# Performance work log

Hardware: AMD Instinct MI355X
Metric: run time of the kernel (lower is better)

The kernel has to match this reference:

```python
import jax, jax.numpy as jnp
import numpy as np
import math

L = 6          # num_layers
D = 512        # hidden_dim
S = 2048       # seq_len
B = 8          # batch
ODIM = 1       # output_dim
SCALES = (24.0, 720.0)


def setup_inputs() -> dict:
    key = jax.random.key(0)
    ks = jax.random.split(key, 12)
    def n(k, shape, scale=0.02):
        return jax.random.normal(k, shape, dtype=jnp.float32) * scale
    return {
        "z": jax.random.normal(ks[0], (B, S, 1), dtype=jnp.float32),
        "c": jax.random.normal(ks[1], (B, S, 1), dtype=jnp.float32),
        "enc_w": n(ks[2], (D, 2)), "enc_b": jnp.zeros((D,), jnp.float32),
        "beta": jnp.ones((L, len(SCALES)), jnp.float32),
        "wq": n(ks[3], (L, D, D)), "bq": jnp.zeros((L, D), jnp.float32),
        "wk": n(ks[4], (L, D, D)), "bk": jnp.zeros((L, D), jnp.float32),
        "wv": n(ks[5], (L, D, D)), "bv": jnp.zeros((L, D), jnp.float32),
        "ln1_w": jnp.ones((L, D), jnp.float32), "ln1_b": jnp.zeros((L, D), jnp.float32),
        "ln2_w": jnp.ones((L, D), jnp.float32), "ln2_b": jnp.zeros((L, D), jnp.float32),
        "ff1_w": n(ks[6], (L, 4 * D, D)), "ff1_b": jnp.zeros((L, 4 * D), jnp.float32),
        "ff2_w": n(ks[7], (L, D, 4 * D)), "ff2_b": jnp.zeros((L, D), jnp.float32),
        "out_w": n(ks[8], (ODIM, D)), "out_b": jnp.zeros((ODIM,), jnp.float32),
    }


def _ln(x, w, b, eps=1e-5):
    m = jnp.mean(x, axis=-1, keepdims=True)
    v = jnp.var(x, axis=-1, keepdims=True)
    return (x - m) * jax.lax.rsqrt(v + eps) * w + b


def _posenc(seq_len, dim):
    pos = jnp.arange(seq_len, dtype=jnp.float32)[:, None]
    div = jnp.exp(jnp.arange(0, dim, 2, dtype=jnp.float32) * (-(math.log(10000.0) / dim)))
    pe = jnp.zeros((seq_len, dim), jnp.float32)
    pe = pe.at[:, 0::2].set(jnp.sin(pos * div))
    pe = pe.at[:, 1::2].set(jnp.cos(pos * div))
    return pe


def reference(z, c, enc_w, enc_b, beta, wq, bq, wk, bk, wv, bv,
              ln1_w, ln1_b, ln2_w, ln2_b, ff1_w, ff1_b, ff2_w, ff2_b,
              out_w, out_b):
    # SequenceEncoder: cat(z,c) -> Linear(2, D) -> + sinusoidal PE
    x = jnp.concatenate([z, c], axis=-1) @ enc_w.T + enc_b       # [B,S,D]
    seq_len, d = x.shape[1], x.shape[2]
    x = x + _posenc(seq_len, d)[None]
    sqrt_d = math.sqrt(d)

    idx = jnp.arange(seq_len, dtype=jnp.float32)
    dist = jnp.abs(idx[:, None] - idx[None, :])                  # [S,S]

    for l in range(L):
        # pre-norm with ln1 (applied twice in the original code - replicated)
        xn = _ln(x, ln1_w[l], ln1_b[l])
        Q = xn @ wq[l].T + bq[l]
        K = xn @ wk[l].T + bk[l]
        V = xn @ wv[l].T + bv[l]
        attn = jnp.einsum('bid,bjd->bij', Q, K) / sqrt_d          # [B,S,S]
        bias = beta[l, 0] * jnp.cos(2.0 * math.pi * dist / SCALES[0]) \
             + beta[l, 1] * jnp.cos(2.0 * math.pi * dist / SCALES[1])
        probs = jax.nn.softmax(attn + bias, axis=-1)
        att_out = jnp.einsum('bij,bjd->bid', probs, V)
        # original applies layer_norm_1 again to the residual sum
        x = _ln(x + att_out, ln1_w[l], ln1_b[l])
        xn2 = _ln(x, ln2_w[l], ln2_b[l])
        h = jax.nn.relu(xn2 @ ff1_w[l].T + ff1_b[l])
        x = x + h @ ff2_w[l].T + ff2_b[l]

    return x @ out_w.T + out_b                                    # [B,S,ODIM]
```

## Files before the change

kernel.cpp:

```cpp
#include <hip/hip_runtime.h>
#include <hip/hip_fp8.h>
#include <math.h>

#define BB 8
#define SS 2048
#define DD 512
#define LL 6
#define FFD 2048

typedef _Float16 half_t;
typedef __attribute__((ext_vector_type(8))) _Float16 half8;
typedef __attribute__((ext_vector_type(4))) float f32x4;

enum { EPI_NONE = 0, EPI_RELU = 2, EPI_RES = 3, EPI_ATTN = 4, EPI_QKV = 5, EPI_PV = 6 };

__device__ __forceinline__ unsigned char f2e4m3(float v) {
    __hip_fp8_e4m3 f(v);
    return f.__x;
}

__device__ __forceinline__ void gl_lds16(const void* g, void* l) {
    __builtin_amdgcn_global_load_lds(
        (const __attribute__((address_space(1))) unsigned int*)g,
        (__attribute__((address_space(3))) unsigned int*)l,
        16, 0, 0);
}

__device__ __forceinline__ void blockReduce2(float& a, float& b, float* sm) {
#pragma unroll
    for (int off = 32; off; off >>= 1) {
        a += __shfl_down(a, off);
        b += __shfl_down(b, off);
    }
    int lane = threadIdx.x & 63;
    int w = threadIdx.x >> 6;
    if (lane == 0) { sm[w] = a; sm[4 + w] = b; }
    __syncthreads();
    a = sm[0] + sm[1] + sm[2] + sm[3];
    b = sm[4] + sm[5] + sm[6] + sm[7];
    __syncthreads();
}

__global__ __launch_bounds__(256) void encode_kernel(
    const float* __restrict__ z, const float* __restrict__ c,
    const float* __restrict__ enc_w, const float* __restrict__ enc_b,
    float* __restrict__ x)
{
    int idx = blockIdx.x * 256 + threadIdx.x;
    int d  = idx & (DD - 1);
    int bs = idx >> 9;
    int s  = bs & (SS - 1);
    float v = z[bs] * enc_w[2 * d] + c[bs] * enc_w[2 * d + 1] + enc_b[d];
    float div = expf(-(float)(d & ~1) * (9.210340371976184f / 512.0f));
    float ang = (float)s * div;
    v += (d & 1) ? cosf(ang) : sinf(ang);
    x[idx] = v;
}

__global__ __launch_bounds__(256) void convert_layer_kernel(
    const float* __restrict__ wq, const float* __restrict__ wk,
    const float* __restrict__ wv, const float* __restrict__ f1,
    const float* __restrict__ f2, half_t* __restrict__ wqkv,
    half_t* __restrict__ f1h, half_t* __restrict__ f2h)
{
    const int NQ = DD * DD;
    int i = blockIdx.x * 256 + threadIdx.x;
    if (i < 3 * NQ) {
        int which = i >> 18, j = i & (NQ - 1);
        const float* s = (which == 0) ? wq : (which == 1) ? wk : wv;
        wqkv[i] = (half_t)s[j];
    } else {
        int k = i - 3 * NQ;
        if (k < FFD * DD) f1h[k] = (half_t)f1[k];
        else              f2h[k - FFD * DD] = (half_t)f2[k - FFD * DD];
    }
}

__global__ __launch_bounds__(256) void bias_table_kernel(
    const float* __restrict__ beta, float* __restrict__ tbl)
{
    int i = blockIdx.x * 256 + threadIdx.x;
    int l = i >> 11, d = i & (SS - 1);
    tbl[i] = beta[2 * l] * cosf(0.2617993877991494f * d)
           + beta[2 * l + 1] * cosf(0.008726646259971648f * d);
}

__global__ __launch_bounds__(256) void ln_kernel(
    const float* __restrict__ src, const float* __restrict__ w,
    const float* __restrict__ b, half_t* __restrict__ dst)
{
    __shared__ float sm[8];
    size_t row = blockIdx.x;
    const float* p = src + row * DD;
    int t = threadIdx.x;
    float v0 = p[t], v1 = p[t + 256];
    float s = v0 + v1, sq = v0 * v0 + v1 * v1;
    blockReduce2(s, sq, sm);
    float mean = s * (1.0f / DD);
    float var  = sq * (1.0f / DD) - mean * mean;
    float rs   = rsqrtf(var + 1e-5f);
    dst[row * DD + t]       = (half_t)((v0 - mean) * rs * w[t] + b[t]);
    dst[row * DD + t + 256] = (half_t)((v1 - mean) * rs * w[t + 256] + b[t + 256]);
}

__global__ __launch_bounds__(256) void ln_ln_kernel(
    float* __restrict__ x,
    const float* __restrict__ w1, const float* __restrict__ b1,
    const float* __restrict__ w2, const float* __restrict__ b2,
    half_t* __restrict__ xn)
{
    __shared__ float sm[8];
    size_t row = blockIdx.x;
    int t = threadIdx.x;
    float v0 = x[row * DD + t];
    float v1 = x[row * DD + t + 256];
    float s = v0 + v1, sq = v0 * v0 + v1 * v1;
    blockReduce2(s, sq, sm);
    float mean = s * (1.0f / DD);
    float var  = sq * (1.0f / DD) - mean * mean;
    float rs   = rsqrtf(var + 1e-5f);
    float y0 = (v0 - mean) * rs * w1[t] + b1[t];
    float y1 = (v1 - mean) * rs * w1[t + 256] + b1[t + 256];
    x[row * DD + t]       = y0;
    x[row * DD + t + 256] = y1;
    s = y0 + y1; sq = y0 * y0 + y1 * y1;
    blockReduce2(s, sq, sm);
    mean = s * (1.0f / DD);
    var  = sq * (1.0f / DD) - mean * mean;
    rs   = rsqrtf(var + 1e-5f);
    xn[row * DD + t]       = (half_t)((y0 - mean) * rs * w2[t] + b2[t]);
    xn[row * DD + t + 256] = (half_t)((y1 - mean) * rs * w2[t + 256] + b2[t + 256]);
}

template<typename TIN, int MT, int EPI, int SWZ = 0>
__global__ __launch_bounds__(256) void gemm_mfma(
    const void* __restrict__ Ap, const void* __restrict__ Wp,
    const float* __restrict__ bias, void* __restrict__ Cp,
    int N, int K, float alpha,
    long long sA, long long sW, long long sC,
    const float* __restrict__ biasK, const float* __restrict__ biasV,
    unsigned char* __restrict__ Ck, unsigned char* __restrict__ Cv)
{
    constexpr int TM = 4;
    constexpr int ES = (int)sizeof(TIN);
    constexpr int NS = (ES == 2) ? 2 : 4;
    constexpr int ABYTES = 128 * 128;
    constexpr int BBYTES = 128 * 128;
    __shared__ __align__(16) unsigned char As[2 * ABYTES];
    __shared__ __align__(16) unsigned char Bs[2 * BBYTES];

    int bxi, byi, bzi;
    if (SWZ == 1) {
        const int id = blockIdx.x;
        const int cc = id & 7, rr = id >> 3;
        bxi = rr & 15;
        const int ss = cc + 8 * (rr >> 4);
        byi = ss & 15; bzi = ss >> 4;
    } else { bxi = blockIdx.x; byi = blockIdx.y; bzi = blockIdx.z; }

    const int z = bzi;
    const unsigned char* A = (const unsigned char*)Ap + (size_t)z * sA * ES;
    const unsigned char* W = (const unsigned char*)Wp + (size_t)z * sW * ES;
    float*  Cf = (float*)Cp  + (size_t)z * sC;
    half_t* Ch = (half_t*)Cp + (size_t)z * sC;
    unsigned char* C8 = (unsigned char*)Cp + (size_t)z * sC;

    const int tid = threadIdx.x;
    const int wv = tid >> 6, ln = tid & 63;
    const int bm = bxi * MT, bn = byi * 128;
    const int wm = (wv & 1) * (MT / 2), wn = (wv >> 1) * 64;

    const int srow  = wv * 32 + (ln >> 3);
    const int scolB = ((ln & 7) ^ ((ln >> 3) & 7)) * 16;
    const unsigned char* Ag = A + (size_t)(bm + srow) * K * ES + scolB;
    const unsigned char* Bg = W + (size_t)(bn + srow) * K * ES + scolB;

    f32x4 acc[TM][4] = {};
    f32x4 accd[TM] = {};
    const long ONES8 = 0x3838383838383838L;

    const int lane15 = ln & 15, quad = ln >> 4;
    const int sw = lane15 & 7;
    const int nIter = (K * ES) / 128;

    auto stage = [&](int b, int t) {
        const size_t ko = (size_t)t * 128;
        unsigned char* la = As + b * ABYTES + wv * 4096;
        unsigned char* lb = Bs + b * BBYTES + wv * 4096;
#pragma unroll
        for (int k = 0; k < 4; ++k) {
            gl_lds16(Ag + (size_t)k * 8 * K * ES + ko, la + k * 1024);
            gl_lds16(Bg + (size_t)k * 8 * K * ES + ko, lb + k * 1024);
        }
    };

    stage(0, 0);
    __syncthreads();

    for (int it = 0; it < nIter; ++it) {
        const int cur = it & 1;
        if (it + 1 < nIter) stage(cur ^ 1, it + 1);

        const unsigned char* Ab = As + cur * ABYTES;
        const unsigned char* Bb = Bs + cur * BBYTES;

        if constexpr (ES == 2) {
#pragma unroll
            for (int s = 0; s < NS; ++s) {
                const int cB = ((s * 4 + quad) ^ sw) * 16;
                half8 aF[TM], bF[4];
#pragma unroll
                for (int i = 0; i < TM; ++i)
                    aF[i] = *(const half8*)(Ab + (wm + i * 16 + lane15) * 128 + cB);
#pragma unroll
                for (int j = 0; j < 4; ++j)
                    bF[j] = *(const half8*)(Bb + (wn + j * 16 + lane15) * 128 + cB);
#pragma unroll
                for (int i = 0; i < TM; ++i)
#pragma unroll
                    for (int j = 0; j < 4; ++j)
                        acc[i][j] = __builtin_amdgcn_mfma_f32_16x16x32_f16(
                            aF[i], bF[j], acc[i][j], 0, 0, 0);
            }
        } else {
#pragma unroll
            for (int s = 0; s < NS; ++s) {
                const int cB = (((s * 2 + (quad >> 1)) ^ sw) * 16) + (quad & 1) * 8;
                long aF8[TM], bF8[4];
#pragma unroll
                for (int i = 0; i < TM; ++i)
                    aF8[i] = *(const long*)(Ab + (wm + i * 16 + lane15) * 128 + cB);
#pragma unroll
                for (int j = 0; j < 4; ++j)
                    bF8[j] = *(const long*)(Bb + (wn + j * 16 + lane15) * 128 + cB);
#pragma unroll
                for (int i = 0; i < TM; ++i) {
#pragma unroll
                    for (int j = 0; j < 4; ++j)
                        acc[i][j] = __builtin_amdgcn_mfma_f32_16x16x32_fp8_fp8(
                            aF8[i], bF8[j], acc[i][j], 0, 0, 0);
                    if (EPI == EPI_PV)
                        accd[i] = __builtin_amdgcn_mfma_f32_16x16x32_fp8_fp8(
                            aF8[i], ONES8, accd[i], 0, 0, 0);
                }
            }
        }

        __syncthreads();
    }

    float invd[TM][4];
    if (EPI == EPI_PV) {
#pragma unroll
        for (int i = 0; i < TM; ++i)
#pragma unroll
            for (int r = 0; r < 4; ++r)
                invd[i][r] = 1.0f / accd[i][r];
    }

#pragma unroll
    for (int i = 0; i < TM; ++i) {
        const int m0 = bm + wm + i * 16 + quad * 4;
#pragma unroll
        for (int j = 0; j < 4; ++j) {
            const int gn = bn + wn + j * 16 + lane15;
            if (EPI == EPI_QKV) {
                const int seg = gn >> 9, nn = gn & (DD - 1);
                if (seg == 2) {
                    unsigned int pk = 0;
#pragma unroll
                    for (int r = 0; r < 4; ++r)
                        pk |= (unsigned int)f2e4m3(acc[i][j][r] + biasV[nn]) << (8 * r);
                    const int b = m0 >> 11, s0 = m0 & (SS - 1);
                    *(unsigned int*)&Cv[((size_t)b * DD + nn) * SS + s0] = pk;
                } else {
                    const float bs = (seg == 0) ? bias[nn] : biasK[nn];
                    unsigned char* dst = (seg == 0) ? C8 : Ck;
#pragma unroll
                    for (int r = 0; r < 4; ++r)
                        dst[(size_t)(m0 + r) * DD + nn] = f2e4m3(acc[i][j][r] + bs);
                }
            } else {
#pragma unroll
                for (int r = 0; r < 4; ++r) {
                    const int gm = m0 + r;
                    float v = acc[i][j][r];
                    if (EPI == EPI_ATTN) {
                        int dist = gm - gn; if (dist < 0) dist = -dist;
                        v = __expf(fminf(v * alpha + bias[dist], 6.0f));
                        C8[(size_t)gm * N + gn] = f2e4m3(v);
                    } else if (EPI == EPI_PV) {
                        const size_t idx = (size_t)gm * N + gn;
                        Cf[idx] = v * invd[i][r] + Cf[idx];
                    } else if (EPI == EPI_RELU) {
                        Ch[(size_t)gm * N + gn] = (half_t)fmaxf(v + bias[gn], 0.0f);
                    } else {
                        const size_t idx = (size_t)gm * N + gn;
                        Cf[idx] = v + bias[gn] + Cf[idx];
                    }
                }
            }
        }
    }
}

__global__ __launch_bounds__(256) void out_kernel(
    const float* __restrict__ x, const float* __restrict__ ow,
    const float* __restrict__ ob, float* __restrict__ out)
{
    int row = blockIdx.x * 4 + (threadIdx.x >> 6);
    int lane = threadIdx.x & 63;
    const float* p = x + (size_t)row * DD;
    float s = 0.f;
#pragma unroll
    for (int k = 0; k < 8; ++k) s += p[lane + 64 * k] * ow[lane + 64 * k];
#pragma unroll
    for (int off = 32; off; off >>= 1) s += __shfl_down(s, off);
    if (lane == 0) out[row] = s + ob[0];
}

extern "C" void kernel_launch(void* const* d_in, const int* in_sizes, int n_in,
                              void* d_out, int out_size, void* d_ws, size_t ws_size,
                              hipStream_t stream)
{
    (void)in_sizes; (void)n_in; (void)out_size; (void)ws_size;
    const float* z     = (const float*)d_in[0];
    const float* c     = (const float*)d_in[1];
    const float* enc_w = (const float*)d_in[2];
    const float* enc_b = (const float*)d_in[3];
    const float* beta  = (const float*)d_in[4];
    const float* wq    = (const float*)d_in[5];
    const float* bq    = (const float*)d_in[6];
    const float* wk    = (const float*)d_in[7];
    const float* bk    = (const float*)d_in[8];
    const float* wv    = (const float*)d_in[9];
    const float* bv    = (const float*)d_in[10];
    const float* ln1w  = (const float*)d_in[11];
    const float* ln1b  = (const float*)d_in[12];
    const float* ln2w  = (const float*)d_in[13];
    const float* ln2b  = (const float*)d_in[14];
    const float* ff1w  = (const float*)d_in[15];
    const float* ff1b  = (const float*)d_in[16];
    const float* ff2w  = (const float*)d_in[17];
    const float* ff2b  = (const float*)d_in[18];
    const float* ow    = (const float*)d_in[19];
    const float* ob    = (const float*)d_in[20];

    const size_t BSD = (size_t)BB * SS * DD;
    const size_t BSS = (size_t)BB * SS * SS;

    char* p = (char*)d_ws;
    float*  x    = (float*)p;  p += BSD * 4;
    half_t* xnh  = (half_t*)p; p += BSD * 2;
    unsigned char* sch = (unsigned char*)p; p += BSS;
    unsigned char* qh  = (unsigned char*)p; p += BSD;
    unsigned char* kh  = (unsigned char*)p; p += BSD;
    unsigned char* vth = (unsigned char*)p; p += BSD;
    half_t* hh   = (half_t*)p; p += (size_t)BB * SS * FFD * 2;
    half_t* wqkv = (half_t*)p; p += (size_t)3 * DD * DD * 2;
    half_t* f1h  = (half_t*)p; p += (size_t)FFD * DD * 2;
    half_t* f2h  = (half_t*)p; p += (size_t)FFD * DD * 2;
    float*  tbl  = (float*)p;

    const float alpha = 0.044194173824159216f;
    const int BS = BB * SS;
    const long long sQ = (long long)SS * DD, sP = (long long)SS * SS,
                    sV = (long long)DD * SS;
    const int CONV_BLKS = (3 * DD * DD + 2 * FFD * DD) / 256;

    bias_table_kernel<<<LL * SS / 256, 256, 0, stream>>>(beta, tbl);
    encode_kernel<<<BS * DD / 256, 256, 0, stream>>>(z, c, enc_w, enc_b, x);

    for (int l = 0; l < LL; ++l) {
        convert_layer_kernel<<<CONV_BLKS, 256, 0, stream>>>(
            wq + (size_t)l * DD * DD, wk + (size_t)l * DD * DD,
            wv + (size_t)l * DD * DD, ff1w + (size_t)l * FFD * DD,
            ff2w + (size_t)l * DD * FFD, wqkv, f1h, f2h);

        ln_kernel<<<BS, 256, 0, stream>>>(x, ln1w + l * DD, ln1b + l * DD, xnh);

        gemm_mfma<half_t, 128, EPI_QKV><<<dim3(BS / 128, 12, 1), 256, 0, stream>>>(
            xnh, wqkv, bq + l * DD, qh, 1536, DD, 0, 0, 0, 0,
            bk + l * DD, bv + l * DD, kh, vth);

        gemm_mfma<unsigned char, 128, EPI_ATTN, 1><<<dim3(2048, 1, 1), 256, 0, stream>>>(
            qh, kh, tbl + l * SS, sch, SS, DD, alpha, sQ, sQ, sP,
            nullptr, nullptr, nullptr, nullptr);

        gemm_mfma<unsigned char, 128, EPI_PV><<<dim3(SS / 128, DD / 128, BB), 256, 0, stream>>>(
            sch, vth, nullptr, x, DD, SS, 0, sP, sV, sQ,
            nullptr, nullptr, nullptr, nullptr);

        ln_ln_kernel<<<BS, 256, 0, stream>>>(x, ln1w + l * DD, ln1b + l * DD,
                                             ln2w + l * DD, ln2b + l * DD, xnh);

        gemm_mfma<half_t, 128, EPI_RELU><<<dim3(BS / 128, FFD / 128, 1), 256, 0, stream>>>(
            xnh, f1h, ff1b + l * FFD, hh, FFD, DD, 0, 0, 0, 0,
            nullptr, nullptr, nullptr, nullptr);
        gemm_mfma<half_t, 128, EPI_RES><<<dim3(BS / 128, DD / 128, 1), 256, 0, stream>>>(
            hh, f2h, ff2b + l * DD, x, DD, FFD, 0, 0, 0, 0,
            nullptr, nullptr, nullptr, nullptr);
    }

    out_kernel<<<BS / 4, 256, 0, stream>>>(x, ow, ob, (float*)d_out);
}
```

Measured before the change: 1.853 ms.

## Replace GEMM with 256-row, 512-thread tiles and interleaved prefetch phases

Replaces the 128x128, 256-thread MFMA GEMM with a template using 256-row tiles, 128- or 256-wide columns and 8 waves per block. Each wave now computes 8 M-fragments, raising arithmetic intensity per LDS load. Global-to-LDS prefetch of the next K-slab is split into phases between MFMA bursts, using explicit barriers, waitcnt and setprio. The goal is more operand reuse and better overlap of loads with compute. The cost is higher register pressure, larger LDS use (up to 128 KB) and fewer blocks for the smaller GEMMs, which can hurt occupancy. The attention swizzle is also rewritten for the new grid.

```diff
diff --git a/kernel.cpp b/kernel.cpp
--- a/kernel.cpp
+++ b/kernel.cpp
@@ -132,8 +132,8 @@
     xn[row * DD + t + 256] = (half_t)((y1 - mean) * rs * w2[t + 256] + b2[t + 256]);
 }
 
-template<typename TIN, int MT, int EPI, int SWZ = 0>
-__global__ __launch_bounds__(256) void gemm_mfma(
+template<typename TIN, int BN, int EPI, int SWZ = 0>
+__global__ __launch_bounds__(512) void gemm256(
     const void* __restrict__ Ap, const void* __restrict__ Wp,
     const float* __restrict__ bias, void* __restrict__ Cp,
     int N, int K, float alpha,
@@ -141,21 +141,20 @@
     const float* __restrict__ biasK, const float* __restrict__ biasV,
     unsigned char* __restrict__ Ck, unsigned char* __restrict__ Cv)
 {
-    constexpr int TM = 4;
-    constexpr int ES = (int)sizeof(TIN);
-    constexpr int NS = (ES == 2) ? 2 : 4;
-    constexpr int ABYTES = 128 * 128;
-    constexpr int BBYTES = 128 * 128;
-    __shared__ __align__(16) unsigned char As[2 * ABYTES];
-    __shared__ __align__(16) unsigned char Bs[2 * BBYTES];
+    constexpr int ES  = (int)sizeof(TIN);
+    constexpr int TN  = BN / 64;
+    constexpr int ASZ = 256 * 128;
+    constexpr int BSZ = BN * 128;
+    constexpr int VM  = 4 + TN;
+    constexpr int PHS = (TN == 4) ? ((ES == 2) ? 4 : 8) : ((ES == 2) ? 2 : 4);
+    __shared__ __align__(16) unsigned char As[2 * ASZ];
+    __shared__ __align__(16) unsigned char Bs[2 * BSZ];
 
     int bxi, byi, bzi;
     if (SWZ == 1) {
         const int id = blockIdx.x;
-        const int cc = id & 7, rr = id >> 3;
-        bxi = rr & 15;
-        const int ss = cc + 8 * (rr >> 4);
-        byi = ss & 15; bzi = ss >> 4;
+        const int ss2 = (id & 7) * 64 + (id >> 3);
+        bxi = ss2 & 7; byi = (ss2 >> 3) & 7; bzi = ss2 >> 6;
     } else { bxi = blockIdx.x; byi = blockIdx.y; bzi = blockIdx.z; }
 
     const int z = bzi;
@@ -167,102 +166,189 @@
 
     const int tid = threadIdx.x;
     const int wv = tid >> 6, ln = tid & 63;
-    const int bm = bxi * MT, bn = byi * 128;
-    const int wm = (wv & 1) * (MT / 2), wn = (wv >> 1) * 64;
-
-    const int srow  = wv * 32 + (ln >> 3);
-    const int scolB = ((ln & 7) ^ ((ln >> 3) & 7)) * 16;
+    const int bm = bxi * 256, bn = byi * BN;
+    const int wm = (wv & 1) * 128, wn = (wv >> 1) * (BN / 4);
+
+    const int srow  = tid >> 3;
+    const int scolB = ((tid & 7) ^ ((tid >> 3) & 7)) * 16;
     const unsigned char* Ag = A + (size_t)(bm + srow) * K * ES + scolB;
     const unsigned char* Bg = W + (size_t)(bn + srow) * K * ES + scolB;
 
-    f32x4 acc[TM][4] = {};
-    f32x4 accd[TM] = {};
+    f32x4 acc[8][TN] = {};
+    f32x4 accd[8] = {};
     const long ONES8 = 0x3838383838383838L;
 
     const int lane15 = ln & 15, quad = ln >> 4;
     const int sw = lane15 & 7;
     const int nIter = (K * ES) / 128;
 
-    auto stage = [&](int b, int t) {
+    auto stageCall = [&](int b, int t, int c) {
         const size_t ko = (size_t)t * 128;
-        unsigned char* la = As + b * ABYTES + wv * 4096;
-        unsigned char* lb = Bs + b * BBYTES + wv * 4096;
-#pragma unroll
-        for (int k = 0; k < 4; ++k) {
-            gl_lds16(Ag + (size_t)k * 8 * K * ES + ko, la + k * 1024);
-            gl_lds16(Bg + (size_t)k * 8 * K * ES + ko, lb + k * 1024);
+        if (c < 4)
+            gl_lds16(Ag + (size_t)(c * 64) * K * ES + ko,
+                     As + b * ASZ + c * 8192 + wv * 1024);
+        else {
+            const int cb = c - 4;
+            gl_lds16(Bg + (size_t)(cb * 64) * K * ES + ko,
+                     Bs + b * BSZ + cb * 8192 + wv * 1024);
         }
     };
 
-    stage(0, 0);
-    __syncthreads();
+#pragma unroll
+    for (int c = 0; c < VM; ++c) stageCall(0, 0, c);
 
     for (int it = 0; it < nIter; ++it) {
         const int cur = it & 1;
-        if (it + 1 < nIter) stage(cur ^ 1, it + 1);
-
-        const unsigned char* Ab = As + cur * ABYTES;
-        const unsigned char* Bb = Bs + cur * BBYTES;
-
-        if constexpr (ES == 2) {
-#pragma unroll
-            for (int s = 0; s < NS; ++s) {
-                const int cB = ((s * 4 + quad) ^ sw) * 16;
-                half8 aF[TM], bF[4];
-#pragma unroll
-                for (int i = 0; i < TM; ++i)
+        asm volatile("s_waitcnt vmcnt(0)" ::: "memory");
+        __builtin_amdgcn_s_barrier();
+
+        const unsigned char* Ab = As + cur * ASZ;
+        const unsigned char* Bb = Bs + cur * BSZ;
+        const bool pf = (it + 1 < nIter);
+
+        if constexpr (ES == 2 && TN == 4) {
+#pragma unroll
+            for (int ks = 0; ks < 2; ++ks) {
+                half8 bF[4];
+#pragma unroll
+                for (int mq = 0; mq < 2; ++mq) {
+                    const int cB = ((ks * 4 + quad) ^ sw) * 16;
+                    half8 aF[4];
+#pragma unroll
+                    for (int i = 0; i < 4; ++i)
+                        aF[i] = *(const half8*)(Ab + (wm + (mq * 4 + i) * 16 + lane15) * 128 + cB);
+                    if (mq == 0)
+#pragma unroll
+                        for (int j = 0; j < 4; ++j)
+                            bF[j] = *(const half8*)(Bb + (wn + j * 16 + lane15) * 128 + cB);
+                    const int p = ks * 2 + mq;
+                    if (pf)
+#pragma unroll
+                        for (int c = p * VM / PHS; c < (p + 1) * VM / PHS; ++c)
+                            stageCall(cur ^ 1, it + 1, c);
+                    __builtin_amdgcn_s_barrier();
+                    asm volatile("s_waitcnt lgkmcnt(0)" ::: "memory");
+                    __builtin_amdgcn_sched_barrier(0);
+                    __builtin_amdgcn_s_setprio(1);
+#pragma unroll
+                    for (int i = 0; i < 4; ++i)
+#pragma unroll
+                        for (int j = 0; j < 4; ++j)
+                            acc[mq * 4 + i][j] = __builtin_amdgcn_mfma_f32_16x16x32_f16(
+                                aF[i], bF[j], acc[mq * 4 + i][j], 0, 0, 0);
+                    __builtin_amdgcn_s_setprio(0);
+                }
+            }
+        } else if constexpr (ES == 2 && TN == 2) {
+#pragma unroll
+            for (int ks = 0; ks < 2; ++ks) {
+                const int cB = ((ks * 4 + quad) ^ sw) * 16;
+                half8 aF[8], bF[2];
+#pragma unroll
+                for (int i = 0; i < 8; ++i)
                     aF[i] = *(const half8*)(Ab + (wm + i * 16 + lane15) * 128 + cB);
 #pragma unroll
-                for (int j = 0; j < 4; ++j)
+                for (int j = 0; j < 2; ++j)
                     bF[j] = *(const half8*)(Bb + (wn + j * 16 + lane15) * 128 + cB);
-#pragma unroll
-                for (int i = 0; i < TM; ++i)
-#pragma unroll
-                    for (int j = 0; j < 4; ++j)
+                const int p = ks;
+                if (pf)
+#pragma unroll
+                    for (int c = p * VM / PHS; c < (p + 1) * VM / PHS; ++c)
+                        stageCall(cur ^ 1, it + 1, c);
+                __builtin_amdgcn_s_barrier();
+                asm volatile("s_waitcnt lgkmcnt(0)" ::: "memory");
+                __builtin_amdgcn_sched_barrier(0);
+                __builtin_amdgcn_s_setprio(1);
+#pragma unroll
+                for (int i = 0; i < 8; ++i)
+#pragma unroll
+                    for (int j = 0; j < 2; ++j)
                         acc[i][j] = __builtin_amdgcn_mfma_f32_16x16x32_f16(
                             aF[i], bF[j], acc[i][j], 0, 0, 0);
+                __builtin_amdgcn_s_setprio(0);
+            }
+        } else if constexpr (ES == 1 && TN == 4) {
+#pragma unroll
+            for (int ks = 0; ks < 4; ++ks) {
+                long bF8[4];
+#pragma unroll
+                for (int mq = 0; mq < 2; ++mq) {
+                    const int cB = (((ks * 2 + (quad >> 1)) ^ sw) * 16) + (quad & 1) * 8;
+                    long aF8[4];
+#pragma unroll
+                    for (int i = 0; i < 4; ++i)
+                        aF8[i] = *(const long*)(Ab + (wm + (mq * 4 + i) * 16 + lane15) * 128 + cB);
+                    if (mq == 0)
+#pragma unroll
+                        for (int j = 0; j < 4; ++j)
+                            bF8[j] = *(const long*)(Bb + (wn + j * 16 + lane15) * 128 + cB);
+                    const int p = ks * 2 + mq;
+                    if (pf)
+#pragma unroll
+                        for (int c = p * VM / PHS; c < (p + 1) * VM / PHS; ++c)
+                            stageCall(cur ^ 1, it + 1, c);
+                    __builtin_amdgcn_s_barrier();
+                    asm volatile("s_waitcnt lgkmcnt(0)" ::: "memory");
+                    __builtin_amdgcn_sched_barrier(0);
+                    __builtin_amdgcn_s_setprio(1);
+#pragma unroll
+                    for (int i = 0; i < 4; ++i)
+#pragma unroll
+                        for (int j = 0; j < 4; ++j)
+                            acc[mq * 4 + i][j] = __builtin_amdgcn_mfma_f32_16x16x32_fp8_fp8(
+                                aF8[i], bF8[j], acc[mq * 4 + i][j], 0, 0, 0);
+                    __builtin_amdgcn_s_setprio(0);
+                }
             }
         } else {
 #pragma unroll
-            for (int s = 0; s < NS; ++s) {
-                const int cB = (((s * 2 + (quad >> 1)) ^ sw) * 16) + (quad & 1) * 8;
-                long aF8[TM], bF8[4];
-#pragma unroll
-                for (int i = 0; i < TM; ++i)
+            for (int ks = 0; ks < 4; ++ks) {
+                const int cB = (((ks * 2 + (quad >> 1)) ^ sw) * 16) + (quad & 1) * 8;
+                long aF8[8], bF8[2];
+#pragma unroll
+                for (int i = 0; i < 8; ++i)
                     aF8[i] = *(const long*)(Ab + (wm + i * 16 + lane15) * 128 + cB);
 #pragma unroll
-                for (int j = 0; j < 4; ++j)
+                for (int j = 0; j < 2; ++j)
                     bF8[j] = *(const long*)(Bb + (wn + j * 16 + lane15) * 128 + cB);
-#pragma unroll
-                for (int i = 0; i < TM; ++i) {
-#pragma unroll
-                    for (int j = 0; j < 4; ++j)
+                const int p = ks;
+                if (pf)
+#pragma unroll
+                    for (int c = p * VM / PHS; c < (p + 1) * VM / PHS; ++c)
+                        stageCall(cur ^ 1, it + 1, c);
+                __builtin_amdgcn_s_barrier();
+                asm volatile("s_waitcnt lgkmcnt(0)" ::: "memory");
+                __builtin_amdgcn_sched_barrier(0);
+                __builtin_amdgcn_s_setprio(1);
+#pragma unroll
+                for (int i = 0; i < 8; ++i) {
+#pragma unroll
+                    for (int j = 0; j < 2; ++j)
                         acc[i][j] = __builtin_amdgcn_mfma_f32_16x16x32_fp8_fp8(
                             aF8[i], bF8[j], acc[i][j], 0, 0, 0);
                     if (EPI == EPI_PV)
                         accd[i] = __builtin_amdgcn_mfma_f32_16x16x32_fp8_fp8(
                             aF8[i], ONES8, accd[i], 0, 0, 0);
                 }
+                __builtin_amdgcn_s_setprio(0);
             }
         }
-
-        __syncthreads();
-    }
-
-    float invd[TM][4];
+    }
+
+    float invd[8][4];
     if (EPI == EPI_PV) {
 #pragma unroll
-        for (int i = 0; i < TM; ++i)
+        for (int i = 0; i < 8; ++i)
 #pragma unroll
             for (int r = 0; r < 4; ++r)
                 invd[i][r] = 1.0f / accd[i][r];
     }
 
 #pragma unroll
-    for (int i = 0; i < TM; ++i) {
+    for (int i = 0; i < 8; ++i) {
         const int m0 = bm + wm + i * 16 + quad * 4;
 #pragma unroll
-        for (int j = 0; j < 4; ++j) {
+        for (int j = 0; j < TN; ++j) {
             const int gn = bn + wn + j * 16 + lane15;
             if (EPI == EPI_QKV) {
                 const int seg = gn >> 9, nn = gn & (DD - 1);
@@ -379,25 +465,25 @@
 
         ln_kernel<<<BS, 256, 0, stream>>>(x, ln1w + l * DD, ln1b + l * DD, xnh);
 
-        gemm_mfma<half_t, 128, EPI_QKV><<<dim3(BS / 128, 12, 1), 256, 0, stream>>>(
+        gemm256<half_t, 128, EPI_QKV><<<dim3(BS / 256, 12, 1), 512, 0, stream>>>(
             xnh, wqkv, bq + l * DD, qh, 1536, DD, 0, 0, 0, 0,
             bk + l * DD, bv + l * DD, kh, vth);
 
-        gemm_mfma<unsigned char, 128, EPI_ATTN, 1><<<dim3(2048, 1, 1), 256, 0, stream>>>(
+        gemm256<unsigned char, 256, EPI_ATTN, 1><<<dim3(512, 1, 1), 512, 0, stream>>>(
             qh, kh, tbl + l * SS, sch, SS, DD, alpha, sQ, sQ, sP,
             nullptr, nullptr, nullptr, nullptr);
 
-        gemm_mfma<unsigned char, 128, EPI_PV><<<dim3(SS / 128, DD / 128, BB), 256, 0, stream>>>(
+        gemm256<unsigned char, 128, EPI_PV><<<dim3(SS / 256, DD / 128, BB), 512, 0, stream>>>(
             sch, vth, nullptr, x, DD, SS, 0, sP, sV, sQ,
             nullptr, nullptr, nullptr, nullptr);
 
         ln_ln_kernel<<<BS, 256, 0, stream>>>(x, ln1w + l * DD, ln1b + l * DD,
                                              ln2w + l * DD, ln2b + l * DD, xnh);
 
-        gemm_mfma<half_t, 128, EPI_RELU><<<dim3(BS / 128, FFD / 128, 1), 256, 0, stream>>>(
+        gemm256<half_t, 256, EPI_RELU><<<dim3(BS / 256, FFD / 256, 1), 512, 0, stream>>>(
             xnh, f1h, ff1b + l * FFD, hh, FFD, DD, 0, 0, 0, 0,
             nullptr, nullptr, nullptr, nullptr);
-        gemm_mfma<half_t, 128, EPI_RES><<<dim3(BS / 128, DD / 128, 1), 256, 0, stream>>>(
+        gemm256<half_t, 128, EPI_RES><<<dim3(BS / 256, DD / 128, 1), 512, 0, stream>>>(
             hh, f2h, ff2b + l * DD, x, DD, FFD, 0, 0, 0, 0,
             nullptr, nullptr, nullptr, nullptr);
     }
```

New measurement: 1.796 ms, median of 2. 3.1% less time.
